# Kernel tuning notes

Measured on AMD Instinct MI355X. Metric: run time of the kernel, lower is better.

The kernel has to match this reference:

```python
import jax, jax.numpy as jnp
import numpy as np

B, T, D, H = 4, 2048, 1024, 16
HD = D // H  # head_dim = 64


def setup_inputs() -> dict:
    key = jax.random.key(0)
    ks = jax.random.split(key, 7)
    x = jax.random.normal(ks[0], (B, T, D), dtype=jnp.float32)
    engagement = jax.random.uniform(ks[1], (B, T), dtype=jnp.float32)
    mask = jax.random.uniform(ks[2], (B, T)) < 0.1  # True = masked-out key
    s = 1.0 / np.sqrt(D)
    qkv_w = jax.random.normal(ks[3], (3 * D, D), dtype=jnp.float32) * s
    qkv_b = jax.random.normal(ks[4], (3 * D,), dtype=jnp.float32) * 0.02
    out_w = jax.random.normal(ks[5], (D, D), dtype=jnp.float32) * s
    out_b = jax.random.normal(ks[6], (D,), dtype=jnp.float32) * 0.02
    return {"x": x, "engagement": engagement, "mask": mask,
            "qkv_w": qkv_w, "qkv_b": qkv_b, "out_w": out_w, "out_b": out_b}


def reference(x, engagement, mask, qkv_w, qkv_b, out_w, out_b):
    b, t, d = x.shape
    qkv = x @ qkv_w.T + qkv_b                       # [B,T,3D]
    q, k, v = jnp.split(qkv, 3, axis=-1)
    # [B,T,D] -> [B,H,T,HD]
    to_heads = lambda a: a.reshape(b, t, H, HD).transpose(0, 2, 1, 3)
    q, k, v = to_heads(q), to_heads(k), to_heads(v)
    attn = jnp.einsum('bhqd,bhkd->bhqk', q, k) / jnp.sqrt(jnp.float32(HD))
    log_g = jnp.log(jnp.clip(engagement, 1e-6))     # [B,T] per-key bias
    attn = attn + log_g[:, None, None, :]
    attn = jnp.where(mask[:, None, None, :], jnp.float32(-1e9), attn)
    p = jax.nn.softmax(attn, axis=-1)
    o = jnp.einsum('bhqk,bhkd->bhqd', p, v)         # [B,H,T,HD]
    o = o.transpose(0, 2, 1, 3).reshape(b, t, d)    # [B,T,D]
    return o @ out_w.T + out_b
```

## Files before the change

kernel.cpp:

```cpp
#include <hip/hip_runtime.h>
#include <math.h>

#define B_  4
#define T_  2048
#define D_  1024
#define H_  16
#define HD_ 64

typedef unsigned short ushort_t;
typedef unsigned int uint_t;
typedef __attribute__((ext_vector_type(8))) short bf16x8;
typedef __attribute__((ext_vector_type(4))) float f32x4;

#define SC_LOG2 0.1803368801111243f

__device__ inline ushort_t f2bf(float f) {
  uint_t u = __float_as_uint(f);
  u += 0x7fffu + ((u >> 16) & 1u);
  return (ushort_t)(u >> 16);
}
__device__ inline ushort_t f2bf_fast(float f) {
  return (ushort_t)((__float_as_uint(f) + 0x8000u) >> 16);
}
__device__ inline uint_t cvtpk_bf16(float lo, float hi) {
  uint_t r;
  asm("v_cvt_pk_bf16_f32 %0, %1, %2" : "=v"(r) : "v"(lo), "v"(hi));
  return r;
}

__device__ inline void gload_lds16(const ushort_t* g, ushort_t* l) {
  __builtin_amdgcn_global_load_lds(
      (const __attribute__((address_space(1))) unsigned int*)g,
      (__attribute__((address_space(3))) unsigned int*)l, 16, 0, 0);
}

__global__ __launch_bounds__(256) void cvt_bf16(const float* __restrict__ in,
                                                ushort_t* __restrict__ out, int n) {
  int i = (blockIdx.x * 256 + threadIdx.x) * 4;
  if (i + 3 < n) {
    float4 v = *(const float4*)(in + i);
    uint_t lo = (uint_t)f2bf(v.x) | ((uint_t)f2bf(v.y) << 16);
    uint_t hi = (uint_t)f2bf(v.z) | ((uint_t)f2bf(v.w) << 16);
    *(uint2*)(out + i) = make_uint2(lo, hi);
  }
}

__global__ __launch_bounds__(256) void bias_prep(const float* __restrict__ eng,
                                                 const int* __restrict__ mask,
                                                 float* __restrict__ biasA, int n) {
  int i = blockIdx.x * 256 + threadIdx.x;
  if (i < n) biasA[i] = mask[i] ? -1e30f : __log2f(fmaxf(eng[i], 1e-6f));
}

template <int WRITE_BF16>
__global__ __launch_bounds__(256) void gemm_bf16(
    const ushort_t* __restrict__ A, const ushort_t* __restrict__ Bm,
    const float* __restrict__ bias, void* __restrict__ Cout,
    int M, int N, int K) {
  __shared__ __align__(16) ushort_t Ls[8192];
  ushort_t* As = Ls;
  ushort_t* Bs = Ls + 4096;
  const int tid = threadIdx.x;
  const int w = tid >> 6, lane = tid & 63;
  const int l15 = lane & 15, quad = lane >> 4;
  const int wm = w >> 1, wn = w & 1;
  const int m0 = blockIdx.y * 128, n0 = blockIdx.x * 128;

  f32x4 acc[4][4];
#pragma unroll
  for (int a = 0; a < 4; ++a)
#pragma unroll
    for (int b = 0; b < 4; ++b) acc[a][b] = (f32x4){0.f, 0.f, 0.f, 0.f};

  const int sr = lane >> 2;
  const int gc = (lane & 3) ^ ((sr >> 1) & 3);

  for (int k0 = 0; k0 < K; k0 += 32) {
    __syncthreads();
#pragma unroll
    for (int u = 0; u < 2; ++u) {
      int row = w * 32 + u * 16 + sr;
      gload_lds16(A + (size_t)(m0 + row) * K + k0 + gc * 8,
                  &As[(w * 32 + u * 16) * 32]);
      gload_lds16(Bm + (size_t)(n0 + row) * K + k0 + gc * 8,
                  &Bs[(w * 32 + u * 16) * 32]);
    }
    __syncthreads();
    bf16x8 af[4], bf[4];
#pragma unroll
    for (int mb = 0; mb < 4; ++mb) {
      int row = wm * 64 + mb * 16 + l15;
      int p = quad ^ ((l15 >> 1) & 3);
      af[mb] = *(const bf16x8*)(&As[row * 32 + p * 8]);
    }
#pragma unroll
    for (int nb = 0; nb < 4; ++nb) {
      int row = wn * 64 + nb * 16 + l15;
      int p = quad ^ ((l15 >> 1) & 3);
      bf[nb] = *(const bf16x8*)(&Bs[row * 32 + p * 8]);
    }
#pragma unroll
    for (int mb = 0; mb < 4; ++mb)
#pragma unroll
      for (int nb = 0; nb < 4; ++nb)
        acc[mb][nb] = __builtin_amdgcn_mfma_f32_16x16x32_bf16(
            af[mb], bf[nb], acc[mb][nb], 0, 0, 0);
  }

  float bb[4];
#pragma unroll
  for (int nb = 0; nb < 4; ++nb) bb[nb] = bias[n0 + wn * 64 + nb * 16 + l15];

  if (WRITE_BF16) {
    ushort_t* Cb = (ushort_t*)Cout;
#pragma unroll
    for (int mb = 0; mb < 4; ++mb) {
      __syncthreads();
#pragma unroll
      for (int nb = 0; nb < 4; ++nb)
#pragma unroll
        for (int i = 0; i < 4; ++i) {
          float v = acc[mb][nb][i] + bb[nb];
          Ls[(wm * 16 + quad * 4 + i) * 136 + wn * 64 + nb * 16 + l15] =
              f2bf_fast(v);
        }
      __syncthreads();
      int lr = tid >> 3, c = tid & 7;
      size_t gr = (size_t)(m0 + (lr >> 4) * 64 + mb * 16 + (lr & 15));
      uint4 v0 = *(const uint4*)&Ls[lr * 136 + c * 16];
      uint4 v1 = *(const uint4*)&Ls[lr * 136 + c * 16 + 8];
      *(uint4*)&Cb[gr * N + n0 + c * 16] = v0;
      *(uint4*)&Cb[gr * N + n0 + c * 16 + 8] = v1;
    }
  } else {
    float* Cf = (float*)Cout;
#pragma unroll
    for (int mb = 0; mb < 4; ++mb)
#pragma unroll
      for (int i = 0; i < 4; ++i) {
        size_t row = (size_t)(m0 + wm * 64 + mb * 16 + quad * 4 + i);
#pragma unroll
        for (int nb = 0; nb < 4; ++nb)
          Cf[row * N + n0 + wn * 64 + nb * 16 + l15] = acc[mb][nb][i] + bb[nb];
      }
  }
}


#define ATTN_TILE(K0, Kc, Vc, bc, Kn, Vn, bn, PF)                              \
  {                                                                            \
    uint4 va_, vc_;                                                            \
    const bool pf_ = (PF);                                                     \
    if (pf_) {                                                                 \
      const int k1_ = (K0) + 64;                                               \
      _Pragma("unroll")                                                        \
      for (int u = 0; u < 2; ++u)                                              \
        gload_lds16(kbase + (size_t)(k1_ + w * 16 + u * 8 + kr) * rs + kgc * 8,\
                    &(Kn)[(w * 16 + u * 8) * 64]);                             \
      const ushort_t* vp_ = vbase + (size_t)(k1_ + 2 * kp) * rs + cc * 8;      \
      va_ = *(const uint4*)vp_;                                                \
      vc_ = *(const uint4*)(vp_ + rs);                                         \
      if (tid < 64) (bn)[tid] = bptr[k1_ + tid];                               \
    }                                                                          \
    bf16x8 kf0[4], kf1[4];                                                     \
    _Pragma("unroll")                                                          \
    for (int nb = 0; nb < 4; ++nb) {                                           \
      int key = nb * 16 + l15;                                                 \
      int p0 = (quad ^ (key & 7)) * 8;                                         \
      kf0[nb] = *(const bf16x8*)(&(Kc)[key * 64 + p0]);                        \
      kf1[nb] = *(const bf16x8*)(&(Kc)[key * 64 + (p0 ^ 32)]);                 \
    }                                                                          \
    bf16x8 vf0[4], vf1[4];                                                     \
    _Pragma("unroll")                                                          \
    for (int nbd = 0; nbd < 4; ++nbd) {                                        \
      vf0[nbd] = *(const bf16x8*)(&(Vc)[quad * 520 + (nbd * 16 + l15) * 8]);   \
      vf1[nbd] =                                                               \
          *(const bf16x8*)(&(Vc)[(4 + quad) * 520 + (nbd * 16 + l15) * 8]);    \
    }                                                                          \
    _Pragma("unroll")                                                          \
    for (int qb = 0; qb < 2; ++qb) {                                           \
      f32x4 st[4];                                                             \
      __builtin_amdgcn_s_setprio(1);                                           \
      _Pragma("unroll")                                                        \
      for (int nb = 0; nb < 4; ++nb) {                                         \
        f32x4 s = (f32x4){0.f, 0.f, 0.f, 0.f};                                 \
        s = __builtin_amdgcn_mfma_f32_16x16x32_bf16(kf0[nb], qf[qb][0], s, 0,  \
                                                    0, 0);                     \
        s = __builtin_amdgcn_mfma_f32_16x16x32_bf16(kf1[nb], qf[qb][1], s, 0,  \
                                                    0, 0);                     \
        st[nb] = s;                                                            \
      }                                                                        \
      __builtin_amdgcn_s_setprio(0);                                           \
      float pp[4][4];                                                          \
      float racc = 0.f;                                                        \
      _Pragma("unroll")                                                        \
      for (int nb = 0; nb < 4; ++nb) {                                         \
        f32x4 bv = *(const f32x4*)&(bc)[nb * 16 + quad * 4];                   \
        _Pragma("unroll")                                                      \
        for (int i = 0; i < 4; ++i) {                                          \
          float p = __builtin_amdgcn_exp2f(st[nb][i] * SC_LOG2 + bv[i]);       \
          pp[nb][i] = p;                                                       \
          racc += p;                                                           \
        }                                                                      \
      }                                                                        \
      rsum[qb] += racc;                                                        \
      union { uint4 u; bf16x8 v; } pf0, pf1;                                   \
      pf0.u.x = cvtpk_bf16(pp[0][0], pp[0][1]);                                \
      pf0.u.y = cvtpk_bf16(pp[0][2], pp[0][3]);                                \
      pf0.u.z = cvtpk_bf16(pp[1][0], pp[1][1]);                                \
      pf0.u.w = cvtpk_bf16(pp[1][2], pp[1][3]);                                \
      pf1.u.x = cvtpk_bf16(pp[2][0], pp[2][1]);                                \
      pf1.u.y = cvtpk_bf16(pp[2][2], pp[2][3]);                                \
      pf1.u.z = cvtpk_bf16(pp[3][0], pp[3][1]);                                \
      pf1.u.w = cvtpk_bf16(pp[3][2], pp[3][3]);                                \
      __builtin_amdgcn_s_setprio(1);                                           \
      _Pragma("unroll")                                                        \
      for (int nbd = 0; nbd < 4; ++nbd) {                                      \
        Oa[qb][nbd] = __builtin_amdgcn_mfma_f32_16x16x32_bf16(                 \
            pf0.v, vf0[nbd], Oa[qb][nbd], 0, 0, 0);                            \
        Oa[qb][nbd] = __builtin_amdgcn_mfma_f32_16x16x32_bf16(                 \
            pf1.v, vf1[nbd], Oa[qb][nbd], 0, 0, 0);                            \
      }                                                                        \
      __builtin_amdgcn_s_setprio(0);                                           \
    }                                                                          \
    if (pf_) {                                                                 \
      uint_t* dst_ = (uint_t*)&(Vn)[gp * 520 + cc * 64 + j0];                  \
      dst_[0]  = (va_.x & 0xffffu) | (vc_.x << 16);                            \
      dst_[4]  = (va_.x >> 16)     | (vc_.x & 0xffff0000u);                    \
      dst_[8]  = (va_.y & 0xffffu) | (vc_.y << 16);                            \
      dst_[12] = (va_.y >> 16)     | (vc_.y & 0xffff0000u);                    \
      dst_[16] = (va_.z & 0xffffu) | (vc_.z << 16);                            \
      dst_[20] = (va_.z >> 16)     | (vc_.z & 0xffff0000u);                    \
      dst_[24] = (va_.w & 0xffffu) | (vc_.w << 16);                            \
      dst_[28] = (va_.w >> 16)     | (vc_.w & 0xffff0000u);                    \
    }                                                                          \
    __syncthreads();                                                           \
  }

__global__ __launch_bounds__(256) void attn_mfma(
    const ushort_t* __restrict__ qkv, const float* __restrict__ biasA,
    ushort_t* __restrict__ oat) {
  __shared__ __align__(16) char smem[34048];
  ushort_t* Kb0 = (ushort_t*)(smem);
  ushort_t* Kb1 = (ushort_t*)(smem + 8192);
  ushort_t* Vb0 = (ushort_t*)(smem + 16384);
  ushort_t* Vb1 = (ushort_t*)(smem + 24704);
  float* bsh0 = (float*)(smem + 33024);
  float* bsh1 = (float*)(smem + 33280);
  float (*lsum)[32] = (float (*)[32])(smem + 33536);

  const int b = blockIdx.z, h = blockIdx.y;
  const int q0 = blockIdx.x * 128;
  const int tid = threadIdx.x;
  const int w = tid >> 6, lane = tid & 63;
  const int l15 = lane & 15, quad = lane >> 4;
  const size_t rs = 3 * D_;

  bf16x8 qf[2][2];
#pragma unroll
  for (int qb = 0; qb < 2; ++qb) {
    const ushort_t* qp =
        qkv + (size_t)(b * T_ + q0 + w * 32 + qb * 16 + l15) * rs + h * HD_;
    qf[qb][0] = *(const bf16x8*)(qp + quad * 8);
    qf[qb][1] = *(const bf16x8*)(qp + 32 + quad * 8);
  }

  f32x4 Oa[2][4];
#pragma unroll
  for (int qb = 0; qb < 2; ++qb)
#pragma unroll
    for (int nb = 0; nb < 4; ++nb) Oa[qb][nb] = (f32x4){0.f, 0.f, 0.f, 0.f};
  float rsum[2] = {0.f, 0.f};

  const ushort_t* kbase = qkv + (size_t)(b * T_) * rs + D_ + h * HD_;
  const ushort_t* vbase = kbase + D_;
  const float* bptr = biasA + b * T_;

  const int kr = lane >> 3, kc = lane & 7;
  const int kgc = kc ^ kr;
  const int kp = tid & 31, cc = tid >> 5;
  const int gp = (kp >> 4) * 4 + ((kp >> 1) & 3);
  const int j0 = ((kp >> 3) & 1) * 4 + 2 * (kp & 1);

  {
#pragma unroll
    for (int u = 0; u < 2; ++u)
      gload_lds16(kbase + (size_t)(w * 16 + u * 8 + kr) * rs + kgc * 8,
                  &Kb0[(w * 16 + u * 8) * 64]);
    const ushort_t* vp = vbase + (size_t)(2 * kp) * rs + cc * 8;
    uint4 va = *(const uint4*)vp;
    uint4 vc = *(const uint4*)(vp + rs);
    if (tid < 64) bsh0[tid] = bptr[tid];
    uint_t* dst = (uint_t*)&Vb0[gp * 520 + cc * 64 + j0];
    dst[0]  = (va.x & 0xffffu) | (vc.x << 16);
    dst[4]  = (va.x >> 16)     | (vc.x & 0xffff0000u);
    dst[8]  = (va.y & 0xffffu) | (vc.y << 16);
    dst[12] = (va.y >> 16)     | (vc.y & 0xffff0000u);
    dst[16] = (va.z & 0xffffu) | (vc.z << 16);
    dst[20] = (va.z >> 16)     | (vc.z & 0xffff0000u);
    dst[24] = (va.w & 0xffffu) | (vc.w << 16);
    dst[28] = (va.w >> 16)     | (vc.w & 0xffff0000u);
  }
  __syncthreads();

  for (int k0 = 0; k0 < T_; k0 += 128) {
    ATTN_TILE(k0,      Kb0, Vb0, bsh0, Kb1, Vb1, bsh1, true);
    ATTN_TILE(k0 + 64, Kb1, Vb1, bsh1, Kb0, Vb0, bsh0, k0 + 128 < T_);
  }

#pragma unroll
  for (int qb = 0; qb < 2; ++qb) {
    float r = rsum[qb];
    r += __shfl_xor(r, 16, 64);
    r += __shfl_xor(r, 32, 64);
    if (lane < 16) lsum[w][qb * 16 + lane] = r;
  }
  ushort_t* OstW = (ushort_t*)(smem) + w * (32 * 72);
#pragma unroll
  for (int qb = 0; qb < 2; ++qb) {
    f32x4 lr = *(const f32x4*)&lsum[w][qb * 16 + quad * 4];
    f32x4 invl;
#pragma unroll
    for (int i = 0; i < 4; ++i) invl[i] = __builtin_amdgcn_rcpf(lr[i]);
#pragma unroll
    for (int nbd = 0; nbd < 4; ++nbd)
#pragma unroll
      for (int i = 0; i < 4; ++i)
        OstW[(qb * 16 + quad * 4 + i) * 72 + nbd * 16 + l15] =
            f2bf_fast(Oa[qb][nbd][i] * invl[i]);
  }
  ushort_t* dst = oat + (size_t)(b * T_ + q0 + w * 32) * D_ + h * HD_;
#pragma unroll
  for (int pp = 0; pp < 4; ++pp) {
    int row = pp * 8 + (lane >> 3), c = lane & 7;
    uint4 v = *(const uint4*)&OstW[row * 72 + c * 8];
    *(uint4*)&dst[(size_t)row * D_ + c * 8] = v;
  }
}

extern "C" void kernel_launch(void* const* d_in, const int* in_sizes, int n_in,
                              void* d_out, int out_size, void* d_ws, size_t ws_size,
                              hipStream_t stream) {
  const float* x     = (const float*)d_in[0];
  const float* eng   = (const float*)d_in[1];
  const int*   mask  = (const int*)d_in[2];
  const float* qkv_w = (const float*)d_in[3];
  const float* qkv_b = (const float*)d_in[4];
  const float* out_w = (const float*)d_in[5];
  const float* out_b = (const float*)d_in[6];
  float* out = (float*)d_out;

  const int M = B_ * T_;
  const size_t nx = (size_t)M * D_;
  const size_t nwq = (size_t)3 * D_ * D_;
  const size_t nwo = (size_t)D_ * D_;
  const size_t nqkv = (size_t)M * 3 * D_;

  char* p = (char*)d_ws;
  ushort_t* xb    = (ushort_t*)p;            p += nx * 2;
  ushort_t* wqkvb = (ushort_t*)p;            p += nwq * 2;
  ushort_t* woutb = (ushort_t*)p;            p += nwo * 2;
  ushort_t* qkvb  = (ushort_t*)p;            p += nqkv * 2;
  ushort_t* oatb  = (ushort_t*)p;            p += nx * 2;
  float*    biasA = (float*)p;               p += (size_t)M * 4;

  cvt_bf16<<<(int)(nx / 1024), 256, 0, stream>>>(x, xb, (int)nx);
  cvt_bf16<<<(int)(nwq / 1024), 256, 0, stream>>>(qkv_w, wqkvb, (int)nwq);
  cvt_bf16<<<(int)(nwo / 1024), 256, 0, stream>>>(out_w, woutb, (int)nwo);
  bias_prep<<<M / 256, 256, 0, stream>>>(eng, mask, biasA, M);

  gemm_bf16<1><<<dim3(3 * D_ / 128, M / 128), 256, 0, stream>>>(
      xb, wqkvb, qkv_b, qkvb, M, 3 * D_, D_);
  attn_mfma<<<dim3(T_ / 128, H_, B_), 256, 0, stream>>>(qkvb, biasA, oatb);
  gemm_bf16<0><<<dim3(D_ / 128, M / 128), 256, 0, stream>>>(
      oatb, woutb, out_b, out, M, D_, D_);
}
```

Before: 321.0 us.

## Replace GEMM with 256x256-tile, 512-thread, 4-stage pipelined kernel

Replaces the 128x128 single-buffered bf16 GEMM with a 256x256-tile kernel of 8 waves. It keeps a 4-slot LDS ring with loads issued 3 chunks ahead, synchronised by explicit vmcnt waits and s_barrier, and raises priority around the MFMA block. It also remaps block IDs in an XCD-aware pattern for L2 locality and rewrites the bf16 epilogue to use per-wave LDS patches. The aim is to hide global-load latency and increase data reuse per tile. In exchange it uses a 128 KB LDS footprint and many more registers, and launches far fewer blocks (128 for the output GEMM), which may underfill the GPU.

```diff
diff --git a/kernel.cpp b/kernel.cpp
--- a/kernel.cpp
+++ b/kernel.cpp
@@ -52,100 +52,128 @@
   if (i < n) biasA[i] = mask[i] ? -1e30f : __log2f(fmaxf(eng[i], 1e-6f));
 }
 
+#define CHUNKS_ 32
+
+#define STAGE_CHUNK(CK, SLOT)                                                  \
+  {                                                                            \
+    const int ck_ = (CK);                                                      \
+    ushort_t* la_ = lds + (SLOT) * 16384 + wA * 32;                            \
+    _Pragma("unroll")                                                          \
+    for (int u = 0; u < 2; ++u) {                                              \
+      gload_lds16(Ag + (size_t)u * 16384 + ck_ * 32, la_ + u * 512);           \
+      gload_lds16(Bg + (size_t)u * 16384 + ck_ * 32, la_ + 8192 + u * 512);    \
+    }                                                                          \
+  }
+
 template <int WRITE_BF16>
-__global__ __launch_bounds__(256) void gemm_bf16(
+__global__ __launch_bounds__(512, 2) void gemm256(
     const ushort_t* __restrict__ A, const ushort_t* __restrict__ Bm,
     const float* __restrict__ bias, void* __restrict__ Cout,
-    int M, int N, int K) {
-  __shared__ __align__(16) ushort_t Ls[8192];
-  ushort_t* As = Ls;
-  ushort_t* Bs = Ls + 4096;
+    int N, int nbx) {
+  __shared__ __align__(16) ushort_t lds[65536];
+
   const int tid = threadIdx.x;
   const int w = tid >> 6, lane = tid & 63;
   const int l15 = lane & 15, quad = lane >> 4;
-  const int wm = w >> 1, wn = w & 1;
-  const int m0 = blockIdx.y * 128, n0 = blockIdx.x * 128;
-
-  f32x4 acc[4][4];
-#pragma unroll
-  for (int a = 0; a < 4; ++a)
-#pragma unroll
-    for (int b = 0; b < 4; ++b) acc[a][b] = (f32x4){0.f, 0.f, 0.f, 0.f};
-
-  const int sr = lane >> 2;
-  const int gc = (lane & 3) ^ ((sr >> 1) & 3);
-
-  for (int k0 = 0; k0 < K; k0 += 32) {
-    __syncthreads();
-#pragma unroll
-    for (int u = 0; u < 2; ++u) {
-      int row = w * 32 + u * 16 + sr;
-      gload_lds16(A + (size_t)(m0 + row) * K + k0 + gc * 8,
-                  &As[(w * 32 + u * 16) * 32]);
-      gload_lds16(Bm + (size_t)(n0 + row) * K + k0 + gc * 8,
-                  &Bs[(w * 32 + u * 16) * 32]);
+  const int wr = w >> 2, wc = w & 3;
+
+  int wg = blockIdx.x;
+  const int cpx = gridDim.x >> 3;
+  wg = (wg & 7) * cpx + (wg >> 3);
+  const int m0 = (wg / nbx) * 256, n0 = (wg % nbx) * 256;
+
+  const int gc = (lane & 3) ^ ((lane >> 3) & 3);
+  const ushort_t* Ag = A + (size_t)(m0 + w * 32 + (lane >> 2)) * 1024 + gc * 8;
+  const ushort_t* Bg = Bm + (size_t)(n0 + w * 32 + (lane >> 2)) * 1024 + gc * 8;
+  const int wA = w * 32;
+
+  const int p8 = (quad ^ ((l15 >> 1) & 3)) * 8;
+  const int rowA = (wr * 128 + l15) * 32 + p8;
+  const int rowB = 8192 + (wc * 64 + l15) * 32 + p8;
+
+  f32x4 acc[8][4];
+#pragma unroll
+  for (int mb = 0; mb < 8; ++mb)
+#pragma unroll
+    for (int nb = 0; nb < 4; ++nb) acc[mb][nb] = (f32x4){0.f, 0.f, 0.f, 0.f};
+
+  STAGE_CHUNK(0, 0);
+  STAGE_CHUNK(1, 1);
+  STAGE_CHUNK(2, 2);
+  asm volatile("s_waitcnt vmcnt(8)" ::: "memory");
+  __builtin_amdgcn_s_barrier();
+  __builtin_amdgcn_sched_barrier(0);
+
+#pragma unroll 1
+  for (int ph = 0; ph < CHUNKS_; ++ph) {
+    const ushort_t* Ls = lds + (ph & 3) * 16384;
+    bf16x8 af[8], bf[4];
+#pragma unroll
+    for (int mb = 0; mb < 8; ++mb)
+      af[mb] = *(const bf16x8*)(Ls + rowA + mb * 512);
+#pragma unroll
+    for (int nb = 0; nb < 4; ++nb)
+      bf[nb] = *(const bf16x8*)(Ls + rowB + nb * 512);
+    if (ph < CHUNKS_ - 3) {
+      STAGE_CHUNK(ph + 3, (ph + 3) & 3);
     }
-    __syncthreads();
-    bf16x8 af[4], bf[4];
-#pragma unroll
-    for (int mb = 0; mb < 4; ++mb) {
-      int row = wm * 64 + mb * 16 + l15;
-      int p = quad ^ ((l15 >> 1) & 3);
-      af[mb] = *(const bf16x8*)(&As[row * 32 + p * 8]);
-    }
-#pragma unroll
-    for (int nb = 0; nb < 4; ++nb) {
-      int row = wn * 64 + nb * 16 + l15;
-      int p = quad ^ ((l15 >> 1) & 3);
-      bf[nb] = *(const bf16x8*)(&Bs[row * 32 + p * 8]);
-    }
-#pragma unroll
-    for (int mb = 0; mb < 4; ++mb)
+    __builtin_amdgcn_s_setprio(1);
+#pragma unroll
+    for (int mb = 0; mb < 8; ++mb)
 #pragma unroll
       for (int nb = 0; nb < 4; ++nb)
         acc[mb][nb] = __builtin_amdgcn_mfma_f32_16x16x32_bf16(
             af[mb], bf[nb], acc[mb][nb], 0, 0, 0);
+    __builtin_amdgcn_s_setprio(0);
+    if (ph < CHUNKS_ - 3)
+      asm volatile("s_waitcnt vmcnt(8)" ::: "memory");
+    else if (ph == CHUNKS_ - 3)
+      asm volatile("s_waitcnt vmcnt(4)" ::: "memory");
+    else
+      asm volatile("s_waitcnt vmcnt(0)" ::: "memory");
+    __builtin_amdgcn_s_barrier();
+    __builtin_amdgcn_sched_barrier(0);
   }
 
   float bb[4];
 #pragma unroll
-  for (int nb = 0; nb < 4; ++nb) bb[nb] = bias[n0 + wn * 64 + nb * 16 + l15];
+  for (int nb = 0; nb < 4; ++nb) bb[nb] = bias[n0 + wc * 64 + nb * 16 + l15];
 
   if (WRITE_BF16) {
+    ushort_t* patch = lds + w * 5120;
     ushort_t* Cb = (ushort_t*)Cout;
 #pragma unroll
-    for (int mb = 0; mb < 4; ++mb) {
-      __syncthreads();
-#pragma unroll
-      for (int nb = 0; nb < 4; ++nb)
-#pragma unroll
-        for (int i = 0; i < 4; ++i) {
-          float v = acc[mb][nb][i] + bb[nb];
-          Ls[(wm * 16 + quad * 4 + i) * 136 + wn * 64 + nb * 16 + l15] =
-              f2bf_fast(v);
-        }
-      __syncthreads();
-      int lr = tid >> 3, c = tid & 7;
-      size_t gr = (size_t)(m0 + (lr >> 4) * 64 + mb * 16 + (lr & 15));
-      uint4 v0 = *(const uint4*)&Ls[lr * 136 + c * 16];
-      uint4 v1 = *(const uint4*)&Ls[lr * 136 + c * 16 + 8];
-      *(uint4*)&Cb[gr * N + n0 + c * 16] = v0;
-      *(uint4*)&Cb[gr * N + n0 + c * 16 + 8] = v1;
+    for (int half = 0; half < 2; ++half) {
+#pragma unroll
+      for (int mb4 = 0; mb4 < 4; ++mb4) {
+#pragma unroll
+        for (int nb = 0; nb < 4; ++nb)
+#pragma unroll
+          for (int i = 0; i < 4; ++i)
+            patch[(mb4 * 16 + quad * 4 + i) * 80 + nb * 16 + l15] =
+                f2bf_fast(acc[half * 4 + mb4][nb][i] + bb[nb]);
+      }
+#pragma unroll
+      for (int it = 0; it < 8; ++it) {
+        int rl = it * 8 + (lane >> 3);
+        size_t grow = (size_t)(m0 + wr * 128 + half * 64 + rl);
+        uint4 v = *(const uint4*)&patch[rl * 80 + (lane & 7) * 8];
+        *(uint4*)&Cb[grow * N + n0 + wc * 64 + (lane & 7) * 8] = v;
+      }
     }
   } else {
     float* Cf = (float*)Cout;
 #pragma unroll
-    for (int mb = 0; mb < 4; ++mb)
+    for (int mb = 0; mb < 8; ++mb)
 #pragma unroll
       for (int i = 0; i < 4; ++i) {
-        size_t row = (size_t)(m0 + wm * 64 + mb * 16 + quad * 4 + i);
+        size_t row = (size_t)(m0 + wr * 128 + mb * 16 + quad * 4 + i);
 #pragma unroll
         for (int nb = 0; nb < 4; ++nb)
-          Cf[row * N + n0 + wn * 64 + nb * 16 + l15] = acc[mb][nb][i] + bb[nb];
+          Cf[row * N + n0 + wc * 64 + nb * 16 + l15] = acc[mb][nb][i] + bb[nb];
       }
   }
 }
-
 
 #define ATTN_TILE(K0, Kc, Vc, bc, Kn, Vn, bn, PF)                              \
   {                                                                            \
@@ -369,9 +397,7 @@
   cvt_bf16<<<(int)(nwo / 1024), 256, 0, stream>>>(out_w, woutb, (int)nwo);
   bias_prep<<<M / 256, 256, 0, stream>>>(eng, mask, biasA, M);
 
-  gemm_bf16<1><<<dim3(3 * D_ / 128, M / 128), 256, 0, stream>>>(
-      xb, wqkvb, qkv_b, qkvb, M, 3 * D_, D_);
+  gemm256<1><<<384, 512, 0, stream>>>(xb, wqkvb, qkv_b, qkvb, 3 * D_, 12);
   attn_mfma<<<dim3(T_ / 128, H_, B_), 256, 0, stream>>>(qkvb, biasA, oatb);
-  gemm_bf16<0><<<dim3(D_ / 128, M / 128), 256, 0, stream>>>(
-      oatb, woutb, out_b, out, M, D_, D_);
-}
+  gemm256<0><<<128, 512, 0, stream>>>(oatb, woutb, out_b, out, D_, 4);
+}
```

Result: no change. 320.5 us (-0.2%).
